# Optimization experiments

Measured on AMD Instinct MI355X. Metric: run time of the kernel, lower is better.

Reference implementation:

```python
import jax, jax.numpy as jnp
import numpy as np

HIDDEN = 2048
N_HEADS = 16
N_KV_HEADS = 4
HEAD_DIM = 128
EPS = 1e-6


def rms_norm(x, w, eps=EPS):
    xf = x.astype(jnp.float32)
    var = jnp.mean(xf * xf, axis=-1, keepdims=True)
    return w * (xf * jax.lax.rsqrt(var + eps)).astype(x.dtype)


def setup_inputs() -> dict:
    key = jax.random.key(0)
    ks = jax.random.split(key, 8)
    B, S, S_ENC = 4, 2048, 1024
    inner = N_HEADS * HEAD_DIM
    kv_dim = N_KV_HEADS * HEAD_DIM
    s = 0.02
    return {
        "hidden_states": jax.random.normal(ks[0], (B, S, HIDDEN), jnp.float32),
        "encoder_hidden_states": jax.random.normal(ks[1], (B, S_ENC, HIDDEN), jnp.float32),
        "Wq": jax.random.normal(ks[2], (HIDDEN, inner), jnp.float32) * s,
        "Wk": jax.random.normal(ks[3], (HIDDEN, kv_dim), jnp.float32) * s,
        "Wv": jax.random.normal(ks[4], (HIDDEN, kv_dim), jnp.float32) * s,
        "Wo": jax.random.normal(ks[5], (inner, HIDDEN), jnp.float32) * s,
        "q_norm_w": jnp.ones((HEAD_DIM,), jnp.float32),
        "k_norm_w": jnp.ones((HEAD_DIM,), jnp.float32),
    }


def reference(hidden_states, encoder_hidden_states, Wq, Wk, Wv, Wo, q_norm_w, k_norm_w):
    B, S, _ = hidden_states.shape
    S_enc = encoder_hidden_states.shape[1]
    groups = N_HEADS // N_KV_HEADS
    scale = 1.0 / (HEAD_DIM ** 0.5)

    q = (hidden_states @ Wq).reshape(B, S, N_HEADS, HEAD_DIM)
    k = (encoder_hidden_states @ Wk).reshape(B, S_enc, N_KV_HEADS, HEAD_DIM)
    v = (encoder_hidden_states @ Wv).reshape(B, S_enc, N_KV_HEADS, HEAD_DIM)

    q = rms_norm(q, q_norm_w)
    k = rms_norm(k, k_norm_w)

    # GQA expand kv heads to full heads
    k = jnp.repeat(k, groups, axis=2)  # [B, S_enc, H, D]
    v = jnp.repeat(v, groups, axis=2)

    # non-causal SDPA
    scores = jnp.einsum("bqhd,bkhd->bhqk", q, k) * scale
    probs = jax.nn.softmax(scores, axis=-1)
    out = jnp.einsum("bhqk,bkhd->bqhd", probs, v)

    out = out.reshape(B, S, N_HEADS * HEAD_DIM)
    return out @ Wo
```

## Files before the change

### kernel.cpp

```cpp
#include <hip/hip_runtime.h>
#include <hip/hip_bf16.h>


typedef short  bf16x8 __attribute__((ext_vector_type(8)));
typedef float  f32x4  __attribute__((ext_vector_type(4)));
typedef unsigned short us;

__device__ __forceinline__ us f2bf(float f) {
    union { float f; unsigned u; } v; v.f = f;
    unsigned r = v.u + 0x7fffu + ((v.u >> 16) & 1u);
    return (us)(r >> 16);
}
__device__ __forceinline__ float bf2f(us u) {
    union { unsigned u; float f; } v; v.u = ((unsigned)u) << 16;
    return v.f;
}

typedef __attribute__((address_space(3))) unsigned int lds_u32;
typedef __attribute__((address_space(1))) const unsigned int glb_u32;

__device__ __forceinline__ void gl_lds16(const us* g, us* l) {
    __builtin_amdgcn_global_load_lds((glb_u32*)g, (lds_u32*)l, 16, 0, 0);
}

__launch_bounds__(256)
__global__ void cvt_kernel(const float* __restrict__ in, us* __restrict__ out) {
    size_t i = ((size_t)blockIdx.x * 256 + threadIdx.x) * 8;
    float4 v0 = *(const float4*)(in + i);
    float4 v1 = *(const float4*)(in + i + 4);
    bf16x8 h;
    h[0] = f2bf(v0.x); h[1] = f2bf(v0.y); h[2] = f2bf(v0.z); h[3] = f2bf(v0.w);
    h[4] = f2bf(v1.x); h[5] = f2bf(v1.y); h[6] = f2bf(v1.z); h[7] = f2bf(v1.w);
    *(bf16x8*)(out + i) = h;
}

__launch_bounds__(256)
__global__ void tpose_kernel(const float* __restrict__ in, us* __restrict__ out,
                             int K, int N) {
    __shared__ us tile[64][65];
    const int n0 = blockIdx.x * 64;
    const int k0 = blockIdx.y * 64;
    const int t  = threadIdx.x;
    const int r  = t >> 4;
    const int c4 = (t & 15) * 4;
    #pragma unroll
    for (int rr = 0; rr < 64; rr += 16) {
        float4 v = *(const float4*)(in + (size_t)(k0 + r + rr) * N + n0 + c4);
        tile[r + rr][c4 + 0] = f2bf(v.x);
        tile[r + rr][c4 + 1] = f2bf(v.y);
        tile[r + rr][c4 + 2] = f2bf(v.z);
        tile[r + rr][c4 + 3] = f2bf(v.w);
    }
    __syncthreads();
    #pragma unroll
    for (int rr = 0; rr < 64; rr += 16) {
        ushort4 o;
        o.x = tile[c4 + 0][r + rr];
        o.y = tile[c4 + 1][r + rr];
        o.z = tile[c4 + 2][r + rr];
        o.w = tile[c4 + 3][r + rr];
        *(ushort4*)(out + (size_t)(n0 + r + rr) * K + k0 + c4) = o;
    }
}

template <int EPI>
__launch_bounds__(256)
__global__ void gemm2_kernel(const us* __restrict__ A,
                             const us* __restrict__ Bt,
                             void* __restrict__ Out,
                             void* __restrict__ Out2,
                             int M, int N, int K) {
    __shared__ __align__(16) us As[128 * 64];
    __shared__ __align__(16) us Bs[128 * 64];

    const int tid  = threadIdx.x;
    const int lane = tid & 63;
    const int wv   = tid >> 6;

    const int nwg  = gridDim.x * gridDim.y;
    const int bid  = blockIdx.y * gridDim.x + blockIdx.x;
    const int cpx  = nwg >> 3;
    const int swz  = (bid & 7) * cpx + (bid >> 3);
    const int row0 = (swz / gridDim.x) * 128;
    const int n0   = (swz % gridDim.x) * 128;

    const int wr   = (wv >> 1) * 64;
    const int wc   = (wv & 1) * 64;
    const int la   = lane & 15;
    const int lg   = lane >> 4;

    const int srow = lane >> 3;
    const int scol = (((lane & 7) ^ srow) * 8);

    const int bs0 = ((0 + lg) ^ (la & 7)) * 8;
    const int bs1 = ((4 + lg) ^ (la & 7)) * 8;

    f32x4 acc[4][4] = {};

    for (int k0 = 0; k0 < K; k0 += 64) {
        #pragma unroll
        for (int r = 0; r < 4; ++r) {
            int brow = wv * 32 + r * 8;
            gl_lds16(Bt + (size_t)(n0 + brow + srow) * K + k0 + scol, &Bs[brow * 64]);
        }
        #pragma unroll
        for (int r = 0; r < 4; ++r) {
            int arow = wv * 32 + r * 8;
            gl_lds16(A + (size_t)(row0 + arow + srow) * K + k0 + scol, &As[arow * 64]);
        }
        __syncthreads();

        bf16x8 af[2][4], bg[2][4];
        #pragma unroll
        for (int i = 0; i < 4; ++i) {
            af[0][i] = *(const bf16x8*)&As[(wr + i * 16 + la) * 64 + bs0];
            af[1][i] = *(const bf16x8*)&As[(wr + i * 16 + la) * 64 + bs1];
        }
        #pragma unroll
        for (int j = 0; j < 4; ++j) {
            bg[0][j] = *(const bf16x8*)&Bs[(wc + j * 16 + la) * 64 + bs0];
            bg[1][j] = *(const bf16x8*)&Bs[(wc + j * 16 + la) * 64 + bs1];
        }
        #pragma unroll
        for (int kk = 0; kk < 2; ++kk)
            #pragma unroll
            for (int i = 0; i < 4; ++i)
                #pragma unroll
                for (int j = 0; j < 4; ++j)
                    acc[i][j] = __builtin_amdgcn_mfma_f32_16x16x32_bf16(af[kk][i], bg[kk][j], acc[i][j], 0, 0, 0);
        __syncthreads();
    }

    const int lgq = lane >> 4;
    #pragma unroll
    for (int i = 0; i < 4; ++i) {
        #pragma unroll
        for (int j = 0; j < 4; ++j) {
            #pragma unroll
            for (int r = 0; r < 4; ++r) {
                int row_g = row0 + wr + i * 16 + lgq * 4 + r;
                int col_g = n0 + wc + j * 16 + la;
                float val = acc[i][j][r];
                if (EPI == 0) {
                    ((us*)Out)[(size_t)row_g * N + col_g] = f2bf(val);
                } else if (EPI == 2) {
                    ((float*)Out)[(size_t)row_g * N + col_g] = val;
                } else {
                    if (col_g < 512) {
                        ((us*)Out)[(size_t)row_g * 512 + col_g] = f2bf(val);
                    } else {
                        int cc  = col_g - 512;
                        int b_  = row_g >> 10, s_ = row_g & 1023;
                        int kvh = cc >> 7,     d_ = cc & 127;
                        ((us*)Out2)[(((size_t)(b_ * 4 + kvh) * 128 + d_) << 10) + s_] = f2bf(val);
                    }
                }
            }
        }
    }
}

__launch_bounds__(256)
__global__ void rmsnorm_kernel(us* __restrict__ x, const float* __restrict__ w,
                               int nseg, float postscale) {
    int seg  = blockIdx.x * 4 + (threadIdx.x >> 6);
    if (seg >= nseg) return;
    int lane = threadIdx.x & 63;
    size_t base = (size_t)seg * 128 + lane * 2;
    unsigned v = *(const unsigned*)&x[base];
    float x0 = bf2f((us)(v & 0xffff));
    float x1 = bf2f((us)(v >> 16));
    float s = x0 * x0 + x1 * x1;
    #pragma unroll
    for (int m = 1; m < 64; m <<= 1) s += __shfl_xor(s, m, 64);
    float rinv = rsqrtf(s * (1.0f / 128.0f) + 1e-6f) * postscale;
    x0 = x0 * rinv * w[lane * 2];
    x1 = x1 * rinv * w[lane * 2 + 1];
    unsigned o = (unsigned)f2bf(x0) | ((unsigned)f2bf(x1) << 16);
    *(unsigned*)&x[base] = o;
}

__launch_bounds__(256, 2)
__global__ void attn_kernel(const us* __restrict__ Q,
                            const us* __restrict__ Kb,
                            const us* __restrict__ Vt,
                            us* __restrict__ Ob) {
    __shared__ __align__(16) us Klds[64 * 132];
    __shared__ __align__(16) us Vtlds[128 * 68];
    __shared__ __align__(16) us Plds[4][32 * 68];

    const int tid  = threadIdx.x;
    const int bid  = blockIdx.x;
    const int qt   = bid & 15;
    const int bh   = bid >> 4;
    const int b    = bh >> 4;
    const int h    = bh & 15;
    const int kvh  = h >> 2;

    const int lane = tid & 63;
    const int wv   = tid >> 6;
    const int la   = lane & 15;
    const int lg   = lane >> 4;
    const int lb   = lg * 8;

    const int qr0 = qt * 128 + wv * 32;

    bf16x8 aq[2][4];
    #pragma unroll
    for (int i = 0; i < 2; ++i)
        #pragma unroll
        for (int t = 0; t < 4; ++t)
            aq[i][t] = *(const bf16x8*)&Q[(size_t)(b * 2048 + qr0 + i * 16 + la) * 2048
                                          + h * 128 + t * 32 + lb];

    f32x4 oacc[2][8] = {};
    float l_part[2][4] = {};

    const us* Kbase  = Kb + (size_t)(b * 1024) * 512 + kvh * 128;
    const us* Vtbase = Vt + (size_t)(b * 4 + kvh) * 128 * 1024;

    for (int kt = 0; kt < 16; ++kt) {
        #pragma unroll
        for (int r = 0; r < 4; ++r) {
            int idx  = tid + r * 256;
            int srow = idx >> 4;
            int c8   = (idx & 15) << 3;
            uint4 v = *(const uint4*)(Kbase + (size_t)(kt * 64 + srow) * 512 + c8);
            *(uint4*)&Klds[srow * 132 + c8] = v;
        }
        #pragma unroll
        for (int r = 0; r < 4; ++r) {
            int idx  = tid + r * 256;
            int drow = idx >> 3;
            int c8   = (idx & 7) << 3;
            uint4 v = *(const uint4*)(Vtbase + (size_t)drow * 1024 + kt * 64 + c8);
            *(uint4*)&Vtlds[drow * 68 + c8] = v;
        }
        __syncthreads();

        f32x4 sacc[2][4] = {};
        __builtin_amdgcn_s_setprio(1);
        #pragma unroll
        for (int j = 0; j < 4; ++j) {
            bf16x8 bk[4];
            #pragma unroll
            for (int t = 0; t < 4; ++t)
                bk[t] = *(const bf16x8*)&Klds[(j * 16 + la) * 132 + t * 32 + lb];
            #pragma unroll
            for (int t = 0; t < 4; ++t)
                #pragma unroll
                for (int i = 0; i < 2; ++i)
                    sacc[i][j] = __builtin_amdgcn_mfma_f32_16x16x32_bf16(aq[i][t], bk[t], sacc[i][j], 0, 0, 0);
        }
        __builtin_amdgcn_s_setprio(0);

        #pragma unroll
        for (int i = 0; i < 2; ++i) {
            #pragma unroll
            for (int r = 0; r < 4; ++r) {
                float ls = 0.0f;
                #pragma unroll
                for (int j = 0; j < 4; ++j) {
                    float p = __builtin_amdgcn_exp2f(sacc[i][j][r]);
                    sacc[i][j][r] = p;
                    ls += p;
                }
                l_part[i][r] += ls;
            }
        }

        #pragma unroll
        for (int i = 0; i < 2; ++i) {
            #pragma unroll
            for (int r = 0; r < 4; ++r) {
                int prow = (i * 16 + lg * 4 + r) * 68;
                #pragma unroll
                for (int j = 0; j < 4; j += 2) {
                    unsigned pk;
                    asm("v_cvt_pk_bf16_f32 %0, %1, %2"
                        : "=v"(pk) : "v"(sacc[i][j][r]), "v"(sacc[i][j + 1][r]));
                    Plds[wv][prow + j * 16 + la]       = (us)(pk & 0xffffu);
                    Plds[wv][prow + (j + 1) * 16 + la] = (us)(pk >> 16);
                }
            }
        }

        __builtin_amdgcn_s_setprio(1);
        #pragma unroll
        for (int ks = 0; ks < 2; ++ks) {
            bf16x8 pa[2];
            #pragma unroll
            for (int i = 0; i < 2; ++i)
                pa[i] = *(const bf16x8*)&Plds[wv][(i * 16 + la) * 68 + ks * 32 + lb];
            #pragma unroll
            for (int df = 0; df < 8; ++df) {
                bf16x8 bv = *(const bf16x8*)&Vtlds[(df * 16 + la) * 68 + ks * 32 + lb];
                #pragma unroll
                for (int i = 0; i < 2; ++i)
                    oacc[i][df] = __builtin_amdgcn_mfma_f32_16x16x32_bf16(pa[i], bv, oacc[i][df], 0, 0, 0);
            }
        }
        __builtin_amdgcn_s_setprio(0);
        __syncthreads();
    }

    #pragma unroll
    for (int i = 0; i < 2; ++i) {
        #pragma unroll
        for (int r = 0; r < 4; ++r) {
            float l = l_part[i][r];
            l += __shfl_xor(l, 1, 64);
            l += __shfl_xor(l, 2, 64);
            l += __shfl_xor(l, 4, 64);
            l += __shfl_xor(l, 8, 64);
            float inv = 1.0f / l;
            int row_g = b * 2048 + qr0 + i * 16 + lg * 4 + r;
            #pragma unroll
            for (int df = 0; df < 8; ++df) {
                int col_g = h * 128 + df * 16 + la;
                Ob[(size_t)row_g * 2048 + col_g] = f2bf(oacc[i][df][r] * inv);
            }
        }
    }
}

extern "C" void kernel_launch(void* const* d_in, const int* in_sizes, int n_in,
                              void* d_out, int out_size, void* d_ws, size_t ws_size,
                              hipStream_t stream) {
    const float* hidden = (const float*)d_in[0];
    const float* enc    = (const float*)d_in[1];
    const float* Wq     = (const float*)d_in[2];
    const float* Wk     = (const float*)d_in[3];
    const float* Wv     = (const float*)d_in[4];
    const float* Wo     = (const float*)d_in[5];
    const float* qw     = (const float*)d_in[6];
    const float* kw     = (const float*)d_in[7];
    float* out = (float*)d_out;

    us* ws16 = (us*)d_ws;
    us* hidden_bf = ws16;
    us* WqT       = ws16 + 16777216;
    us* Qu        = ws16 + 20971520;
    us* enc_bf    = ws16;
    us* WkT       = ws16 + 8388608;
    us* WvT       = ws16 + 9437184;
    us* WoT       = ws16 + 10485760;
    us* Kn        = ws16 + 14680064;
    us* Vt        = ws16 + 16777216;

    dim3 blk(256);
    const float qscale = 0.08838834764831845f * 1.4426950408889634f;

    cvt_kernel<<<dim3(8192), blk, 0, stream>>>(hidden, hidden_bf);
    tpose_kernel<<<dim3(32, 32), blk, 0, stream>>>(Wq, WqT, 2048, 2048);
    gemm2_kernel<0><<<dim3(16, 64), blk, 0, stream>>>(hidden_bf, WqT, Qu, nullptr, 8192, 2048, 2048);

    cvt_kernel<<<dim3(4096), blk, 0, stream>>>(enc, enc_bf);
    tpose_kernel<<<dim3(8, 32),  blk, 0, stream>>>(Wk, WkT, 2048, 512);
    tpose_kernel<<<dim3(8, 32),  blk, 0, stream>>>(Wv, WvT, 2048, 512);
    tpose_kernel<<<dim3(32, 32), blk, 0, stream>>>(Wo, WoT, 2048, 2048);
    gemm2_kernel<3><<<dim3(8, 32), blk, 0, stream>>>(enc_bf, WkT, Kn, Vt, 4096, 1024, 2048);

    rmsnorm_kernel<<<dim3(32768), blk, 0, stream>>>(Qu, qw, 8192 * 16, qscale);
    rmsnorm_kernel<<<dim3(4096),  blk, 0, stream>>>(Kn, kw, 4096 * 4, 1.0f);

    attn_kernel<<<dim3(1024), blk, 0, stream>>>(Qu, Kn, Vt, Qu);

    gemm2_kernel<2><<<dim3(16, 64), blk, 0, stream>>>(Qu, WoT, out, nullptr, 8192, 2048, 2048);
}
```

Baseline: 367.5 us.

## Add 256x256 double-buffered 8-wave GEMM for Q and output projections

Adds a new GEMM kernel with 256x256 tiles and 512 threads. It double-buffers A and B tiles in LDS using direct global-to-LDS loads that are interleaved with MFMA phases, and uses s_setprio plus explicit barriers and waitcnts. The new kernel replaces the 128x128 single-buffered GEMM for the Q projection and the output projection. The aim is more data reuse per tile and overlap of global loads with compute, at the cost of much more LDS per block (about 128KB), fewer blocks in flight, and fragile synchronisation.

```diff
diff --git a/kernel.cpp b/kernel.cpp
--- a/kernel.cpp
+++ b/kernel.cpp
@@ -63,6 +63,168 @@
     }
 }
 
+#define G3_BAR  __builtin_amdgcn_s_barrier()
+#define G3_LGKM asm volatile("s_waitcnt lgkmcnt(0)" ::: "memory")
+#define G3_SB0  __builtin_amdgcn_sched_barrier(0)
+
+template <int EPI>
+__launch_bounds__(512, 2)
+__global__ void gemm3_kernel(const us* __restrict__ A,
+                             const us* __restrict__ Bt,
+                             void* __restrict__ Out,
+                             int M, int N, int K) {
+    __shared__ __align__(16) us As[2][2][128 * 64];
+    __shared__ __align__(16) us Bs[2][2][128 * 64];
+
+    const int tid  = threadIdx.x;
+    const int lane = tid & 63;
+    const int w    = tid >> 6;
+    const int wrow = w >> 2;
+    const int wcol = w & 3;
+
+    const int nwg  = gridDim.x * gridDim.y;
+    const int bid  = blockIdx.y * gridDim.x + blockIdx.x;
+    const int cpx  = nwg >> 3;
+    const int swz  = (bid & 7) * cpx + (bid >> 3);
+    const int row0 = (swz / gridDim.x) * 256;
+    const int n0   = (swz % gridDim.x) * 256;
+
+    const int la = lane & 15;
+    const int lg = lane >> 4;
+    const int sr = lane >> 3;
+    const int sc = ((lane & 7) ^ sr) * 8;
+    const int bs0 = ((0 + lg) ^ (la & 7)) * 8;
+    const int bs1 = ((4 + lg) ^ (la & 7)) * 8;
+
+    const int nkt = K >> 6;
+
+#define STAGE_A(rb, k0_, dst)                                                   \
+    {                                                                           \
+        _Pragma("unroll")                                                       \
+        for (int g = 0; g < 2; ++g) {                                           \
+            int r_ = w * 16 + g * 8;                                            \
+            gl_lds16(A + (size_t)((rb) + r_ + sr) * K + (k0_) + sc,             \
+                     &(dst)[r_ * 64]);                                          \
+        }                                                                       \
+    }
+#define STAGE_B(cn, k0_)                                                        \
+    {                                                                           \
+        us* dsth_ = &Bs[(cn)][w >> 2][0];                                       \
+        _Pragma("unroll")                                                       \
+        for (int g = 0; g < 4; ++g) {                                           \
+            int r_ = (w & 3) * 32 + g * 8;                                      \
+            gl_lds16(Bt + (size_t)(n0 + (w >> 2) * 128 + r_ + sr) * K           \
+                         + (k0_) + sc,                                          \
+                     &dsth_[r_ * 64]);                                          \
+        }                                                                       \
+    }
+
+    f32x4 acc[8][4] = {};
+
+    STAGE_A(row0,        0, As[0][0]);
+    STAGE_A(row0 + 128,  0, As[0][1]);
+    STAGE_B(0, 0);
+    STAGE_A(row0,       64, As[1][0]);
+    STAGE_A(row0 + 128, 64, As[1][1]);
+    asm volatile("s_waitcnt vmcnt(0)" ::: "memory");
+    __syncthreads();
+
+    bf16x8 af[8][2], bg[2][2];
+
+    for (int t = 0; t < nkt; ++t) {
+        const int c  = t & 1;
+        const int cn = c ^ 1;
+        const int k0 = t << 6;
+        const us* Ar = &As[c][wrow][0];
+        const us* Br = &Bs[c][wcol >> 1][0];
+        const int brow = (wcol & 1) * 64;
+
+        #pragma unroll
+        for (int rf = 0; rf < 8; ++rf) {
+            af[rf][0] = *(const bf16x8*)&Ar[(rf * 16 + la) * 64 + bs0];
+            af[rf][1] = *(const bf16x8*)&Ar[(rf * 16 + la) * 64 + bs1];
+        }
+        #pragma unroll
+        for (int j = 0; j < 2; ++j) {
+            bg[j][0] = *(const bf16x8*)&Br[(brow + j * 16 + la) * 64 + bs0];
+            bg[j][1] = *(const bf16x8*)&Br[(brow + j * 16 + la) * 64 + bs1];
+        }
+        if (t + 1 < nkt) STAGE_B(cn, k0 + 64);
+        G3_BAR; G3_LGKM; G3_SB0;
+        __builtin_amdgcn_s_setprio(1);
+        #pragma unroll
+        for (int rf = 0; rf < 4; ++rf)
+            #pragma unroll
+            for (int j = 0; j < 2; ++j) {
+                acc[rf][j] = __builtin_amdgcn_mfma_f32_16x16x32_bf16(af[rf][0], bg[j][0], acc[rf][j], 0, 0, 0);
+                acc[rf][j] = __builtin_amdgcn_mfma_f32_16x16x32_bf16(af[rf][1], bg[j][1], acc[rf][j], 0, 0, 0);
+            }
+        __builtin_amdgcn_s_setprio(0);
+        G3_BAR;
+
+        if (t + 2 < nkt) STAGE_A(row0, k0 + 128, As[c][0]);
+        G3_BAR;
+        __builtin_amdgcn_s_setprio(1);
+        #pragma unroll
+        for (int rf = 4; rf < 8; ++rf)
+            #pragma unroll
+            for (int j = 0; j < 2; ++j) {
+                acc[rf][j] = __builtin_amdgcn_mfma_f32_16x16x32_bf16(af[rf][0], bg[j][0], acc[rf][j], 0, 0, 0);
+                acc[rf][j] = __builtin_amdgcn_mfma_f32_16x16x32_bf16(af[rf][1], bg[j][1], acc[rf][j], 0, 0, 0);
+            }
+        __builtin_amdgcn_s_setprio(0);
+        G3_BAR;
+
+        #pragma unroll
+        for (int j = 0; j < 2; ++j) {
+            bg[j][0] = *(const bf16x8*)&Br[(brow + (2 + j) * 16 + la) * 64 + bs0];
+            bg[j][1] = *(const bf16x8*)&Br[(brow + (2 + j) * 16 + la) * 64 + bs1];
+        }
+        if (t + 2 < nkt) STAGE_A(row0 + 128, k0 + 128, As[c][1]);
+        G3_BAR; G3_LGKM; G3_SB0;
+        __builtin_amdgcn_s_setprio(1);
+        #pragma unroll
+        for (int rf = 0; rf < 4; ++rf)
+            #pragma unroll
+            for (int j = 0; j < 2; ++j) {
+                acc[rf][2 + j] = __builtin_amdgcn_mfma_f32_16x16x32_bf16(af[rf][0], bg[j][0], acc[rf][2 + j], 0, 0, 0);
+                acc[rf][2 + j] = __builtin_amdgcn_mfma_f32_16x16x32_bf16(af[rf][1], bg[j][1], acc[rf][2 + j], 0, 0, 0);
+            }
+        __builtin_amdgcn_s_setprio(0);
+        G3_BAR;
+
+        __builtin_amdgcn_s_setprio(1);
+        #pragma unroll
+        for (int rf = 4; rf < 8; ++rf)
+            #pragma unroll
+            for (int j = 0; j < 2; ++j) {
+                acc[rf][2 + j] = __builtin_amdgcn_mfma_f32_16x16x32_bf16(af[rf][0], bg[j][0], acc[rf][2 + j], 0, 0, 0);
+                acc[rf][2 + j] = __builtin_amdgcn_mfma_f32_16x16x32_bf16(af[rf][1], bg[j][1], acc[rf][2 + j], 0, 0, 0);
+            }
+        __builtin_amdgcn_s_setprio(0);
+        if (t >= nkt - 2) { asm volatile("s_waitcnt vmcnt(0)" ::: "memory"); }
+        else              { asm volatile("s_waitcnt vmcnt(2)" ::: "memory"); }
+        G3_BAR;
+    }
+
+    #pragma unroll
+    for (int rf = 0; rf < 8; ++rf) {
+        #pragma unroll
+        for (int cf = 0; cf < 4; ++cf) {
+            #pragma unroll
+            for (int rr = 0; rr < 4; ++rr) {
+                int row_g = row0 + wrow * 128 + rf * 16 + lg * 4 + rr;
+                int col_g = n0 + wcol * 64 + cf * 16 + la;
+                float val = acc[rf][cf][rr];
+                if (EPI == 0) ((us*)Out)[(size_t)row_g * N + col_g] = f2bf(val);
+                else          ((float*)Out)[(size_t)row_g * N + col_g] = val;
+            }
+        }
+    }
+}
+#undef STAGE_A
+#undef STAGE_B
+
 template <int EPI>
 __launch_bounds__(256)
 __global__ void gemm2_kernel(const us* __restrict__ A,
@@ -91,7 +253,6 @@
 
     const int srow = lane >> 3;
     const int scol = (((lane & 7) ^ srow) * 8);
-
     const int bs0 = ((0 + lg) ^ (la & 7)) * 8;
     const int bs1 = ((4 + lg) ^ (la & 7)) * 8;
 
@@ -131,14 +292,13 @@
         __syncthreads();
     }
 
-    const int lgq = lane >> 4;
     #pragma unroll
     for (int i = 0; i < 4; ++i) {
         #pragma unroll
         for (int j = 0; j < 4; ++j) {
             #pragma unroll
             for (int r = 0; r < 4; ++r) {
-                int row_g = row0 + wr + i * 16 + lgq * 4 + r;
+                int row_g = row0 + wr + i * 16 + lg * 4 + r;
                 int col_g = n0 + wc + j * 16 + la;
                 float val = acc[i][j][r];
                 if (EPI == 0) {
@@ -353,7 +513,7 @@
 
     cvt_kernel<<<dim3(8192), blk, 0, stream>>>(hidden, hidden_bf);
     tpose_kernel<<<dim3(32, 32), blk, 0, stream>>>(Wq, WqT, 2048, 2048);
-    gemm2_kernel<0><<<dim3(16, 64), blk, 0, stream>>>(hidden_bf, WqT, Qu, nullptr, 8192, 2048, 2048);
+    gemm3_kernel<0><<<dim3(8, 32), dim3(512), 0, stream>>>(hidden_bf, WqT, Qu, 8192, 2048, 2048);
 
     cvt_kernel<<<dim3(4096), blk, 0, stream>>>(enc, enc_bf);
     tpose_kernel<<<dim3(8, 32),  blk, 0, stream>>>(Wk, WkT, 2048, 512);
@@ -366,5 +526,5 @@
 
     attn_kernel<<<dim3(1024), blk, 0, stream>>>(Qu, Kn, Vt, Qu);
 
-    gemm2_kernel<2><<<dim3(16, 64), blk, 0, stream>>>(Qu, WoT, out, nullptr, 8192, 2048, 2048);
-}
+    gemm3_kernel<2><<<dim3(8, 32), dim3(512), 0, stream>>>(Qu, WoT, out, 8192, 2048, 2048);
+}
```

Result: faster. 329.0 us (-10.5%).
